# Kernel optimization log

Measured on AMD Instinct MI355X. Metric: run time of the kernel, lower is better.

Reference implementation:

```python
import jax, jax.numpy as jnp
import numpy as np

INPUT_DIMS = 512
OUTPUT_DIMS = 512
DEGREE = 7
ALPHA = 1.0


def setup_inputs() -> dict:
    key = jax.random.key(0)
    k1, k2 = jax.random.split(key)
    x = jax.random.normal(k1, (16384, INPUT_DIMS), dtype=jnp.float32)
    std = 1.0 / (INPUT_DIMS * (DEGREE + 1))
    coeffs = jax.random.normal(k2, (INPUT_DIMS, OUTPUT_DIMS, DEGREE + 1), dtype=jnp.float32) * std
    return {"x": x, "gegenbauer_coeffs": coeffs}


def reference(x, gegenbauer_coeffs):
    # x: (B, I) -> tanh squashed into (-1, 1) domain of Gegenbauer polys
    x = jnp.tanh(x.reshape(-1, INPUT_DIMS))
    a = ALPHA
    polys = [jnp.ones_like(x)]
    if DEGREE > 0:
        polys.append(2.0 * a * x)
    # recurrence: C_{n+1} = (2(n+a) x C_n - (n+2a-1) C_{n-1}) / (n+1)
    for n in range(1, DEGREE):
        polys.append((2.0 * (n + a) * x * polys[n] - (n + 2.0 * a - 1.0) * polys[n - 1]) / (n + 1.0))
    g = jnp.stack(polys, axis=-1)  # (B, I, D+1)
    y = jnp.einsum('bid,iod->bo', g, gegenbauer_coeffs)
    return y.reshape(-1, OUTPUT_DIMS)
```

## Files before the change

### kernel.cpp

```cpp
#include <hip/hip_runtime.h>
#include <hip/hip_bf16.h>


#define I_DIM 512
#define O_DIM 512
#define NDEG 8
#define BM 128
#define BN 128
#define IPB 8
#define LSTR 72
#define KITERS (I_DIM / IPB)
#define NTHREADS 256
#define W_ELEMS (I_DIM * O_DIM * NDEG)

typedef __attribute__((ext_vector_type(8))) short s8v;
typedef __attribute__((ext_vector_type(4))) float f32x4;
typedef unsigned short u16;

__device__ __forceinline__ unsigned pack2bf(float a, float b) {
    unsigned ua = __float_as_uint(a), ub = __float_as_uint(b);
    ua += 0x7fffu + ((ua >> 16) & 1u);
    ub += 0x7fffu + ((ub >> 16) & 1u);
    return (ua >> 16) | (ub & 0xffff0000u);
}

__device__ __forceinline__ float fast_tanh(float v) {
    float e = __expf(v + v);
    float r = __builtin_amdgcn_rcpf(e + 1.0f);
    return 1.0f - (r + r);
}

extern "C" __global__ __launch_bounds__(256)
void cvt_w(const float* __restrict__ cf, u16* __restrict__ wbf) {
    const size_t idx = ((size_t)blockIdx.x * 256 + threadIdx.x) * 4;
    const float4 v = *reinterpret_cast<const float4*>(cf + idx);
    unsigned* dst = reinterpret_cast<unsigned*>(wbf + idx);
    dst[0] = pack2bf(v.x, v.y);
    dst[1] = pack2bf(v.z, v.w);
}

template <bool PRECONV>
__global__ __launch_bounds__(NTHREADS, 4)
void gegen_gemm(const float* __restrict__ x,
                const float* __restrict__ cf,
                const u16* __restrict__ wbf,
                float* __restrict__ out)
{
    __shared__ u16 As[BM * LSTR];
    __shared__ u16 Ws[IPB * BN * NDEG];

    const int tid  = threadIdx.x;
    const int lane = tid & 63;
    const int wave = tid >> 6;
    const int fm   = lane & 15;
    const int fq   = lane >> 4;
    const int wr   = (wave >> 1) << 6;
    const int wc   = (wave & 1) << 6;

    const int bm0 = blockIdx.y * BM;
    const int bn0 = blockIdx.x * BN;

    const int ar = tid >> 1;
    const int ai = (tid & 1) << 2;
    const float* xp = x + (size_t)(bm0 + ar) * I_DIM + ai;

    f32x4 acc[4][4];
#pragma unroll
    for (int a = 0; a < 4; ++a)
#pragma unroll
        for (int b = 0; b < 4; ++b)
            acc[a][b] = (f32x4){0.0f, 0.0f, 0.0f, 0.0f};

    for (int it = 0; it < KITERS; ++it) {
        if (PRECONV) {
            const u16* wsrc = wbf + ((size_t)(it * IPB) * O_DIM + bn0) * NDEG;
#pragma unroll
            for (int q = 0; q < 4; ++q) {
                const int c    = wave * 4 + q;
                const int il   = c >> 1;
                const int half = c & 1;
                const u16* src = wsrc + ((size_t)il * O_DIM + half * 64 + lane) * NDEG;
                u16* dst = &Ws[(il * BN + half * 64) * NDEG];
                __builtin_amdgcn_global_load_lds(
                    (const __attribute__((address_space(1))) void*)src,
                    (__attribute__((address_space(3))) void*)dst, 16, 0, 0);
            }
        } else {
#pragma unroll
            for (int jj = 0; jj < 4; ++jj) {
                const int p  = jj * NTHREADS + tid;
                const int il = p >> 7;
                const int o  = p & 127;
                const float* src = cf + ((size_t)(it * IPB + il) * O_DIM + bn0 + o) * NDEG;
                const float4 w0 = reinterpret_cast<const float4*>(src)[0];
                const float4 w1 = reinterpret_cast<const float4*>(src)[1];
                union { s8v s; unsigned u[4]; } pk;
                pk.u[0] = pack2bf(w0.x, w0.y);
                pk.u[1] = pack2bf(w0.z, w0.w);
                pk.u[2] = pack2bf(w1.x, w1.y);
                pk.u[3] = pack2bf(w1.z, w1.w);
                *reinterpret_cast<s8v*>(&Ws[(il * BN + o) * NDEG]) = pk.s;
            }
        }

        {
            const float4 xv = *reinterpret_cast<const float4*>(xp + it * IPB);
            const float vv[4] = {xv.x, xv.y, xv.z, xv.w};
#pragma unroll
            for (int j = 0; j < 4; ++j) {
                const float t  = fast_tanh(vv[j]);
                const float t2 = t + t;
                const float c1 = t2;
                const float c2 = t2 * c1 - 1.0f;
                const float c3 = t2 * c2 - c1;
                const float c4 = t2 * c3 - c2;
                const float c5 = t2 * c4 - c3;
                const float c6 = t2 * c5 - c4;
                const float c7 = t2 * c6 - c5;
                union { s8v s; unsigned u[4]; } pk;
                pk.u[0] = pack2bf(1.0f, c1);
                pk.u[1] = pack2bf(c2, c3);
                pk.u[2] = pack2bf(c4, c5);
                pk.u[3] = pack2bf(c6, c7);
                *reinterpret_cast<s8v*>(&As[ar * LSTR + (ai + j) * NDEG]) = pk.s;
            }
        }
        __syncthreads();

#pragma unroll
        for (int kc = 0; kc < 2; ++kc) {
            s8v afr[4], bfr[4];
#pragma unroll
            for (int tm = 0; tm < 4; ++tm)
                afr[tm] = *reinterpret_cast<const s8v*>(
                    &As[(wr + tm * 16 + fm) * LSTR + kc * 32 + fq * 8]);
#pragma unroll
            for (int tn = 0; tn < 4; ++tn)
                bfr[tn] = *reinterpret_cast<const s8v*>(
                    &Ws[((kc * 4 + fq) * BN + wc + tn * 16 + fm) * NDEG]);
#pragma unroll
            for (int tm = 0; tm < 4; ++tm)
#pragma unroll
                for (int tn = 0; tn < 4; ++tn)
                    acc[tm][tn] = __builtin_amdgcn_mfma_f32_16x16x32_bf16(
                        afr[tm], bfr[tn], acc[tm][tn], 0, 0, 0);
        }
        __syncthreads();
    }

#pragma unroll
    for (int tm = 0; tm < 4; ++tm) {
#pragma unroll
        for (int tn = 0; tn < 4; ++tn) {
            const int row = bm0 + wr + tm * 16 + fq * 4;
            const int col = bn0 + wc + tn * 16 + fm;
#pragma unroll
            for (int r = 0; r < 4; ++r)
                out[(size_t)(row + r) * O_DIM + col] = acc[tm][tn][r];
        }
    }
}

extern "C" void kernel_launch(void* const* d_in, const int* in_sizes, int n_in,
                              void* d_out, int out_size, void* d_ws, size_t ws_size,
                              hipStream_t stream) {
    const float* x  = (const float*)d_in[0];
    const float* cf = (const float*)d_in[1];
    float* out = (float*)d_out;
    const int M = in_sizes[0] / I_DIM;
    dim3 grid(O_DIM / BN, M / BM);
    dim3 block(NTHREADS, 1, 1);

    if (ws_size >= (size_t)W_ELEMS * sizeof(u16)) {
        u16* wbf = (u16*)d_ws;
        cvt_w<<<W_ELEMS / 1024, 256, 0, stream>>>(cf, wbf);
        gegen_gemm<true><<<grid, block, 0, stream>>>(x, cf, wbf, out);
    } else {
        gegen_gemm<false><<<grid, block, 0, stream>>>(x, cf, nullptr, out);
    }
}
```

Baseline: 172.4 us.

## Drop LDS staging; load MFMA fragments directly from global with register prefetch

Removes shared-memory tiles and block barriers. Each wave now loads its A inputs (raw x pairs) and B fragments (from a pre-transposed, k-permuted bf16 weight layout produced by cvt_w) straight from global memory into registers, double-buffering the next iteration's loads. The polynomial expansion is computed per wave right before the MFMAs, so no data is shared between waves. This trades LDS traffic and sync stalls for redundant global/L2 loads and duplicated tanh/recurrence work, and lowers the occupancy hint to 2 blocks per SIMD group.

```diff
diff --git a/kernel.cpp b/kernel.cpp
--- a/kernel.cpp
+++ b/kernel.cpp
@@ -5,19 +5,14 @@
 #define I_DIM 512
 #define O_DIM 512
 #define NDEG 8
-#define BM 128
-#define BN 128
-#define IPB 8
-#define LSTR 72
-#define KITERS (I_DIM / IPB)
-#define NTHREADS 256
-#define W_ELEMS (I_DIM * O_DIM * NDEG)
-
-typedef __attribute__((ext_vector_type(8))) short s8v;
-typedef __attribute__((ext_vector_type(4))) float f32x4;
+#define K_DIM (I_DIM * NDEG)
+#define W_BYTES ((size_t)O_DIM * K_DIM * sizeof(unsigned short))
+
+typedef short s8v __attribute__((ext_vector_type(8)));
+typedef float f32x4 __attribute__((ext_vector_type(4)));
 typedef unsigned short u16;
 
-__device__ __forceinline__ unsigned pack2bf(float a, float b) {
+__device__ __forceinline__ unsigned pack2bf_rne(float a, float b) {
     unsigned ua = __float_as_uint(a), ub = __float_as_uint(b);
     ua += 0x7fffu + ((ua >> 16) & 1u);
     ub += 0x7fffu + ((ub >> 16) & 1u);
@@ -30,39 +25,67 @@
     return 1.0f - (r + r);
 }
 
+__device__ __forceinline__ s8v cheb_frag(float t) {
+    const float t2 = t + t;
+    const float c1 = t2;
+    const float c2 = t2 * c1 - 1.0f;
+    const float c3 = t2 * c2 - c1;
+    const float c4 = t2 * c3 - c2;
+    const float c5 = t2 * c4 - c3;
+    const float c6 = t2 * c5 - c4;
+    const float c7 = t2 * c6 - c5;
+    union { s8v s; __hip_bfloat162 h[4]; } pk;
+    pk.h[0] = __float22bfloat162_rn(make_float2(1.0f, c1));
+    pk.h[1] = __float22bfloat162_rn(make_float2(c2, c3));
+    pk.h[2] = __float22bfloat162_rn(make_float2(c4, c5));
+    pk.h[3] = __float22bfloat162_rn(make_float2(c6, c7));
+    return pk.s;
+}
+
 extern "C" __global__ __launch_bounds__(256)
-void cvt_w(const float* __restrict__ cf, u16* __restrict__ wbf) {
-    const size_t idx = ((size_t)blockIdx.x * 256 + threadIdx.x) * 4;
-    const float4 v = *reinterpret_cast<const float4*>(cf + idx);
-    unsigned* dst = reinterpret_cast<unsigned*>(wbf + idx);
-    dst[0] = pack2bf(v.x, v.y);
-    dst[1] = pack2bf(v.z, v.w);
+void cvt_w(const float* __restrict__ cf, u16* __restrict__ wt) {
+    const int idx = blockIdx.x * 256 + threadIdx.x;
+    const int q = idx & (I_DIM - 1);
+    const int o = idx >> 9;
+    const int i = (q & ~7) | ((q & 3) << 1) | ((q >> 2) & 1);
+    const float* src = cf + ((size_t)i * O_DIM + o) * NDEG;
+    const float4 w0 = reinterpret_cast<const float4*>(src)[0];
+    const float4 w1 = reinterpret_cast<const float4*>(src)[1];
+    union { s8v s; unsigned u[4]; } pk;
+    pk.u[0] = pack2bf_rne(w0.x, w0.y);
+    pk.u[1] = pack2bf_rne(w0.z, w0.w);
+    pk.u[2] = pack2bf_rne(w1.x, w1.y);
+    pk.u[3] = pack2bf_rne(w1.z, w1.w);
+    *reinterpret_cast<s8v*>(wt + (size_t)o * K_DIM + q * NDEG) = pk.s;
 }
 
 template <bool PRECONV>
-__global__ __launch_bounds__(NTHREADS, 4)
+__global__ __launch_bounds__(256, 2)
 void gegen_gemm(const float* __restrict__ x,
                 const float* __restrict__ cf,
-                const u16* __restrict__ wbf,
+                const u16* __restrict__ wt,
                 float* __restrict__ out)
 {
-    __shared__ u16 As[BM * LSTR];
-    __shared__ u16 Ws[IPB * BN * NDEG];
-
     const int tid  = threadIdx.x;
     const int lane = tid & 63;
     const int wave = tid >> 6;
     const int fm   = lane & 15;
     const int fq   = lane >> 4;
-    const int wr   = (wave >> 1) << 6;
-    const int wc   = (wave & 1) << 6;
-
-    const int bm0 = blockIdx.y * BM;
-    const int bn0 = blockIdx.x * BN;
-
-    const int ar = tid >> 1;
-    const int ai = (tid & 1) << 2;
-    const float* xp = x + (size_t)(bm0 + ar) * I_DIM + ai;
+
+    const int m0 = blockIdx.y * 256 + wave * 64;
+    const int n0 = blockIdx.x * 64;
+
+    const float* xb[4];
+#pragma unroll
+    for (int tm = 0; tm < 4; ++tm)
+        xb[tm] = x + (size_t)(m0 + tm * 16 + fm) * I_DIM + 2 * fq;
+    const u16* wb[4];
+    const float* cb[4];
+#pragma unroll
+    for (int tn = 0; tn < 4; ++tn) {
+        wb[tn] = wt + (size_t)(n0 + tn * 16 + fm) * K_DIM + fq * NDEG;
+        cb[tn] = cf + (size_t)(n0 + tn * 16 + fm) * NDEG;
+    }
 
     f32x4 acc[4][4];
 #pragma unroll
@@ -71,94 +94,93 @@
         for (int b = 0; b < 4; ++b)
             acc[a][b] = (f32x4){0.0f, 0.0f, 0.0f, 0.0f};
 
-    for (int it = 0; it < KITERS; ++it) {
-        if (PRECONV) {
-            const u16* wsrc = wbf + ((size_t)(it * IPB) * O_DIM + bn0) * NDEG;
-#pragma unroll
-            for (int q = 0; q < 4; ++q) {
-                const int c    = wave * 4 + q;
-                const int il   = c >> 1;
-                const int half = c & 1;
-                const u16* src = wsrc + ((size_t)il * O_DIM + half * 64 + lane) * NDEG;
-                u16* dst = &Ws[(il * BN + half * 64) * NDEG];
-                __builtin_amdgcn_global_load_lds(
-                    (const __attribute__((address_space(1))) void*)src,
-                    (__attribute__((address_space(3))) void*)dst, 16, 0, 0);
+    float2 xv[4];
+    s8v    bfr[2][4];
+
+#pragma unroll
+    for (int tm = 0; tm < 4; ++tm)
+        xv[tm] = *reinterpret_cast<const float2*>(xb[tm]);
+#pragma unroll
+    for (int kc = 0; kc < 2; ++kc)
+#pragma unroll
+        for (int tn = 0; tn < 4; ++tn) {
+            if (PRECONV) {
+                bfr[kc][tn] = *reinterpret_cast<const s8v*>(wb[tn] + kc * 32);
+            } else {
+                const int i = 2 * fq + kc;
+                const float* p = cb[tn] + (size_t)i * O_DIM * NDEG;
+                const float4 w0 = reinterpret_cast<const float4*>(p)[0];
+                const float4 w1 = reinterpret_cast<const float4*>(p)[1];
+                union { s8v s; unsigned u[4]; } pk;
+                pk.u[0] = pack2bf_rne(w0.x, w0.y);
+                pk.u[1] = pack2bf_rne(w0.z, w0.w);
+                pk.u[2] = pack2bf_rne(w1.x, w1.y);
+                pk.u[3] = pack2bf_rne(w1.z, w1.w);
+                bfr[kc][tn] = pk.s;
             }
-        } else {
-#pragma unroll
-            for (int jj = 0; jj < 4; ++jj) {
-                const int p  = jj * NTHREADS + tid;
-                const int il = p >> 7;
-                const int o  = p & 127;
-                const float* src = cf + ((size_t)(it * IPB + il) * O_DIM + bn0 + o) * NDEG;
-                const float4 w0 = reinterpret_cast<const float4*>(src)[0];
-                const float4 w1 = reinterpret_cast<const float4*>(src)[1];
-                union { s8v s; unsigned u[4]; } pk;
-                pk.u[0] = pack2bf(w0.x, w0.y);
-                pk.u[1] = pack2bf(w0.z, w0.w);
-                pk.u[2] = pack2bf(w1.x, w1.y);
-                pk.u[3] = pack2bf(w1.z, w1.w);
-                *reinterpret_cast<s8v*>(&Ws[(il * BN + o) * NDEG]) = pk.s;
-            }
-        }
-
-        {
-            const float4 xv = *reinterpret_cast<const float4*>(xp + it * IPB);
-            const float vv[4] = {xv.x, xv.y, xv.z, xv.w};
-#pragma unroll
-            for (int j = 0; j < 4; ++j) {
-                const float t  = fast_tanh(vv[j]);
-                const float t2 = t + t;
-                const float c1 = t2;
-                const float c2 = t2 * c1 - 1.0f;
-                const float c3 = t2 * c2 - c1;
-                const float c4 = t2 * c3 - c2;
-                const float c5 = t2 * c4 - c3;
-                const float c6 = t2 * c5 - c4;
-                const float c7 = t2 * c6 - c5;
-                union { s8v s; unsigned u[4]; } pk;
-                pk.u[0] = pack2bf(1.0f, c1);
-                pk.u[1] = pack2bf(c2, c3);
-                pk.u[2] = pack2bf(c4, c5);
-                pk.u[3] = pack2bf(c6, c7);
-                *reinterpret_cast<s8v*>(&As[ar * LSTR + (ai + j) * NDEG]) = pk.s;
-            }
-        }
-        __syncthreads();
+        }
+
+    for (int it = 0; it < K_DIM / 64; ++it) {
+        float2 xn[4];
+        s8v    bn[2][4];
+        if (it < K_DIM / 64 - 1) {
+            const int nit = it + 1;
+#pragma unroll
+            for (int tm = 0; tm < 4; ++tm)
+                xn[tm] = *reinterpret_cast<const float2*>(xb[tm] + nit * NDEG);
+#pragma unroll
+            for (int kc = 0; kc < 2; ++kc)
+#pragma unroll
+                for (int tn = 0; tn < 4; ++tn) {
+                    if (PRECONV) {
+                        bn[kc][tn] = *reinterpret_cast<const s8v*>(wb[tn] + nit * 64 + kc * 32);
+                    } else {
+                        const int i = nit * NDEG + 2 * fq + kc;
+                        const float* p = cb[tn] + (size_t)i * O_DIM * NDEG;
+                        const float4 w0 = reinterpret_cast<const float4*>(p)[0];
+                        const float4 w1 = reinterpret_cast<const float4*>(p)[1];
+                        union { s8v s; unsigned u[4]; } pk;
+                        pk.u[0] = pack2bf_rne(w0.x, w0.y);
+                        pk.u[1] = pack2bf_rne(w0.z, w0.w);
+                        pk.u[2] = pack2bf_rne(w1.x, w1.y);
+                        pk.u[3] = pack2bf_rne(w1.z, w1.w);
+                        bn[kc][tn] = pk.s;
+                    }
+                }
+        }
 
 #pragma unroll
         for (int kc = 0; kc < 2; ++kc) {
-            s8v afr[4], bfr[4];
+            s8v afr[4];
 #pragma unroll
             for (int tm = 0; tm < 4; ++tm)
-                afr[tm] = *reinterpret_cast<const s8v*>(
-                    &As[(wr + tm * 16 + fm) * LSTR + kc * 32 + fq * 8]);
-#pragma unroll
-            for (int tn = 0; tn < 4; ++tn)
-                bfr[tn] = *reinterpret_cast<const s8v*>(
-                    &Ws[((kc * 4 + fq) * BN + wc + tn * 16 + fm) * NDEG]);
+                afr[tm] = cheb_frag(fast_tanh(kc ? xv[tm].y : xv[tm].x));
 #pragma unroll
             for (int tm = 0; tm < 4; ++tm)
 #pragma unroll
                 for (int tn = 0; tn < 4; ++tn)
                     acc[tm][tn] = __builtin_amdgcn_mfma_f32_16x16x32_bf16(
-                        afr[tm], bfr[tn], acc[tm][tn], 0, 0, 0);
-        }
-        __syncthreads();
+                        afr[tm], bfr[kc][tn], acc[tm][tn], 0, 0, 0);
+        }
+
+#pragma unroll
+        for (int tm = 0; tm < 4; ++tm) xv[tm] = xn[tm];
+#pragma unroll
+        for (int kc = 0; kc < 2; ++kc)
+#pragma unroll
+            for (int tn = 0; tn < 4; ++tn) bfr[kc][tn] = bn[kc][tn];
     }
 
 #pragma unroll
-    for (int tm = 0; tm < 4; ++tm) {
+    for (int tm = 0; tm < 4; ++tm)
 #pragma unroll
         for (int tn = 0; tn < 4; ++tn) {
-            const int row = bm0 + wr + tm * 16 + fq * 4;
-            const int col = bn0 + wc + tn * 16 + fm;
+            const int row = m0 + tm * 16 + fq * 4;
+            const int col = n0 + tn * 16 + fm;
 #pragma unroll
             for (int r = 0; r < 4; ++r)
                 out[(size_t)(row + r) * O_DIM + col] = acc[tm][tn][r];
         }
-    }
 }
 
 extern "C" void kernel_launch(void* const* d_in, const int* in_sizes, int n_in,
@@ -168,13 +190,13 @@
     const float* cf = (const float*)d_in[1];
     float* out = (float*)d_out;
     const int M = in_sizes[0] / I_DIM;
-    dim3 grid(O_DIM / BN, M / BM);
-    dim3 block(NTHREADS, 1, 1);
-
-    if (ws_size >= (size_t)W_ELEMS * sizeof(u16)) {
-        u16* wbf = (u16*)d_ws;
-        cvt_w<<<W_ELEMS / 1024, 256, 0, stream>>>(cf, wbf);
-        gegen_gemm<true><<<grid, block, 0, stream>>>(x, cf, wbf, out);
+    dim3 grid(O_DIM / 64, M / 256);
+    dim3 block(256, 1, 1);
+
+    if (ws_size >= W_BYTES) {
+        u16* wt = (u16*)d_ws;
+        cvt_w<<<(I_DIM * O_DIM) / 256, 256, 0, stream>>>(cf, wt);
+        gegen_gemm<true><<<grid, block, 0, stream>>>(x, cf, wt, out);
     } else {
         gegen_gemm<false><<<grid, block, 0, stream>>>(x, cf, nullptr, out);
     }
```

Result: slower. 257.5 us (+49.3%).
